# Kernel tuning notes

Hardware: AMD Instinct MI355X
Metric: run time of the kernel (lower is better)

Reference implementation:

```python
import jax, jax.numpy as jnp
import numpy as np

CAPACITY_FACTOR = 1.0  # fairseq Top1Gate default


def setup_inputs() -> dict:
    key = jax.random.key(0)
    ks = jax.random.split(key, 5)
    B, T, M, H, O, E = 8, 1024, 1024, 4096, 1024, 4
    return {
        "hidden_states": jax.random.normal(ks[0], (B, T, M), jnp.float32),
        "gate_w": jax.random.normal(ks[1], (M, E), jnp.float32) * 0.02,
        "fc1_w": jax.random.normal(ks[2], (E, M, H), jnp.float32) * 0.02,
        "fc1_b": jnp.zeros((E, H), jnp.float32),
        "fc2_w": jax.random.normal(ks[3], (E, H, O), jnp.float32) * 0.02,
        "fc2_b": jnp.zeros((E, O), jnp.float32),
    }


def reference(hidden_states, gate_w, fc1_w, fc1_b, fc2_w, fc2_b):
    B, T, M = hidden_states.shape
    E = gate_w.shape[1]
    S = B * T
    C = int(CAPACITY_FACTOR * -(-S // E))  # ceil(S/E)

    features = hidden_states.reshape(S, M)  # [S, M]

    # ---- Top1 gate (fairseq top1gating, eval path: no shuffle/noise) ----
    logits = features @ gate_w                      # [S, E]
    gates = jax.nn.softmax(logits, axis=1)          # [S, E]
    idx = jnp.argmax(gates, axis=1)                 # [S]
    mask1 = jax.nn.one_hot(idx, E, dtype=gates.dtype)  # [S, E]

    # load-balancing aux loss (computed before capacity dropping)
    me = jnp.mean(gates, axis=0)
    ce = jnp.mean(mask1, axis=0)
    l_aux = jnp.sum(me * ce) * E

    # capacity: position within each expert's queue; drop overflow tokens
    locations = jnp.cumsum(mask1, axis=0) - 1.0     # [S, E]
    mask1 = mask1 * (locations < C)
    loc_s = jnp.sum(locations * mask1, axis=1).astype(jnp.int32)  # [S]
    gates1_s = jnp.sum(gates * mask1, axis=1)       # [S] gate value (0 if dropped)

    # combine_weights [S, E, C] and boolean dispatch mask (as float for mm)
    combine = (gates1_s[:, None, None] * mask1[:, :, None]
               * jax.nn.one_hot(loc_s, C, dtype=gates.dtype)[:, None, :])
    dispatch = (combine > 0).astype(features.dtype)  # [S, E, C]

    # ---- dispatch via dense one-hot matmul: [E*C, S] @ [S, M] ----
    dispatch_ecs = jnp.transpose(dispatch, (1, 2, 0)).reshape(E * C, S)
    dispatched = (dispatch_ecs @ features).reshape(E, C, M)

    # ---- per-expert MLP (grouped GEMM) ----
    h = jax.nn.gelu(jnp.einsum('ecm,emh->ech', dispatched, fc1_w) + fc1_b[:, None, :])
    expert_out = jnp.einsum('ech,eho->eco', h, fc2_w) + fc2_b[:, None, :]  # [E, C, O]

    # ---- combine via dense matmul: [S, E*C] @ [E*C, O] ----
    O = expert_out.shape[-1]
    combined = combine.reshape(S, E * C) @ expert_out.reshape(E * C, O)

    return combined.reshape(B, T, O), l_aux
```

## Files before the change

### kernel.cpp

```cpp
#include <hip/hip_runtime.h>
#include <stdint.h>

#define S_TOK 8192
#define MDIM  1024
#define HDIM  4096
#define ODIM  1024
#define NEXP  4
#define CAP   2048

typedef __attribute__((ext_vector_type(8))) short short8;
typedef __attribute__((ext_vector_type(4))) float floatx4;

__device__ __forceinline__ unsigned short f2bf(float x) {
  union { float f; unsigned u; } v; v.f = x;
  unsigned r = v.u + 0x7FFFu + ((v.u >> 16) & 1u);
  return (unsigned short)(r >> 16);
}

__device__ __forceinline__ void gl_lds16(const void* g, void* l) {
  __builtin_amdgcn_global_load_lds(
      (const __attribute__((address_space(1))) void*)g,
      (__attribute__((address_space(3))) void*)l, 16, 0, 0);
}

__device__ __forceinline__ float gelu_tanh(float x) {
  float z = 0.7978845608028654f * (x + 0.044715f * x * x * x);
  float t = 1.0f - 2.0f / (__expf(2.0f * z) + 1.0f);
  return 0.5f * x * (1.0f + t);
}

__global__ __launch_bounds__(256) void gate_kernel(
    const float* __restrict__ feat, const float* __restrict__ gw,
    int* __restrict__ idx, float* __restrict__ gval, float* __restrict__ gsum)
{
  int wave = threadIdx.x >> 6, lane = threadIdx.x & 63;
  int s = blockIdx.x * 4 + wave;
  const float* f = feat + (size_t)s * MDIM;
  double a0 = 0, a1 = 0, a2 = 0, a3 = 0;
  #pragma unroll
  for (int j = 0; j < 16; ++j) {
    int m = lane + j * 64;
    float x = f[m];
    float4 w = ((const float4*)gw)[m];
    a0 += (double)x * w.x; a1 += (double)x * w.y;
    a2 += (double)x * w.z; a3 += (double)x * w.w;
  }
  #pragma unroll
  for (int off = 32; off; off >>= 1) {
    a0 += __shfl_down(a0, off); a1 += __shfl_down(a1, off);
    a2 += __shfl_down(a2, off); a3 += __shfl_down(a3, off);
  }
  __shared__ float bs[4];
  if (threadIdx.x < 4) bs[threadIdx.x] = 0.f;
  __syncthreads();
  if (lane == 0) {
    double lg[4] = {a0, a1, a2, a3};
    double mx = lg[0]; int bi = 0;
    #pragma unroll
    for (int e = 1; e < 4; ++e) if (lg[e] > mx) { mx = lg[e]; bi = e; }
    float ex[4]; float den = 0.f;
    #pragma unroll
    for (int e = 0; e < 4; ++e) { ex[e] = __expf((float)(lg[e] - mx)); den += ex[e]; }
    float inv = 1.f / den;
    idx[s]  = bi;
    gval[s] = ex[bi] * inv;
    #pragma unroll
    for (int e = 0; e < 4; ++e) atomicAdd(&bs[e], ex[e] * inv);
  }
  __syncthreads();
  if (threadIdx.x < 4) atomicAdd(&gsum[threadIdx.x], bs[threadIdx.x]);
}

__global__ __launch_bounds__(1024) void scan_kernel(
    const int* __restrict__ idx, int* __restrict__ perm,
    int* __restrict__ ne, const float* __restrict__ gsum,
    float* __restrict__ laux)
{
  const int tid = threadIdx.x, wave = tid >> 6, lane = tid & 63;
  __shared__ int cnt[16][4];
  __shared__ int off[16][4];
  __shared__ int tot[4];
  unsigned long long below = (lane == 0) ? 0ull : ((~0ull) >> (64 - lane));

  int myE[8], loc[8];
  int c[4] = {0, 0, 0, 0};
  #pragma unroll
  for (int j = 0; j < 8; ++j) {
    int s = wave * 512 + j * 64 + lane;
    int ev = idx[s];
    myE[j] = ev;
    #pragma unroll
    for (int e = 0; e < 4; ++e) {
      unsigned long long mb = __ballot(ev == e);
      if (ev == e) loc[j] = c[e] + __popcll(mb & below);
      c[e] += __popcll(mb);
    }
  }
  if (lane == 0) {
    #pragma unroll
    for (int e = 0; e < 4; ++e) cnt[wave][e] = c[e];
  }
  __syncthreads();
  if (tid < 64) {
    int w = tid >> 2, e = tid & 3;
    int o = 0;
    for (int w2 = 0; w2 < 16; ++w2) if (w2 < w) o += cnt[w2][e];
    off[w][e] = o;
    if (w == 15) tot[e] = o + cnt[15][e];
  }
  __syncthreads();
  #pragma unroll
  for (int j = 0; j < 8; ++j) {
    int s = wave * 512 + j * 64 + lane;
    int e = myE[j];
    int rank = off[wave][e] + loc[j];
    if (rank < CAP) perm[e * CAP + rank] = s;
  }
  if (tid < 4) ne[tid] = tot[tid] < CAP ? tot[tid] : CAP;
  if (tid == 0) {
    float l = 0.f;
    #pragma unroll
    for (int e = 0; e < 4; ++e)
      l += (gsum[e] * (1.0f / S_TOK)) * ((float)tot[e] * (1.0f / S_TOK));
    *laux = l * (float)NEXP;
  }
}

__global__ __launch_bounds__(256) void transpose_cast(
    const float* __restrict__ in, unsigned short* __restrict__ out, int R, int Cc)
{
  __shared__ unsigned short tile[64][66];
  in  += (size_t)blockIdx.z * R * Cc;
  out += (size_t)blockIdx.z * R * Cc;
  int c0 = blockIdx.x * 64, r0 = blockIdx.y * 64;
  int tx = threadIdx.x & 15;
  int ty = threadIdx.x >> 4;
  #pragma unroll
  for (int p = 0; p < 4; ++p) {
    int r = ty + p * 16;
    float4 v = *(const float4*)(in + (size_t)(r0 + r) * Cc + c0 + tx * 4);
    tile[r][tx * 4 + 0] = f2bf(v.x);
    tile[r][tx * 4 + 1] = f2bf(v.y);
    tile[r][tx * 4 + 2] = f2bf(v.z);
    tile[r][tx * 4 + 3] = f2bf(v.w);
  }
  __syncthreads();
  #pragma unroll
  for (int p = 0; p < 4; ++p) {
    int c = ty + p * 16;
    ushort4 o;
    o.x = tile[tx * 4 + 0][c];
    o.y = tile[tx * 4 + 1][c];
    o.z = tile[tx * 4 + 2][c];
    o.w = tile[tx * 4 + 3][c];
    *(ushort4*)(out + (size_t)(c0 + c) * R + r0 + tx * 4) = o;
  }
}

__global__ __launch_bounds__(256) void gather_kernel(
    const float* __restrict__ feat, const int* __restrict__ perm,
    const int* __restrict__ ne, unsigned short* __restrict__ disp)
{
  int b = blockIdx.x;
  int e = b >> 11, c = b & (CAP - 1);
  int m = threadIdx.x * 4;
  ushort4 o;
  if (c < ne[e]) {
    int s = perm[b];
    float4 v = *(const float4*)(feat + (size_t)s * MDIM + m);
    o.x = f2bf(v.x); o.y = f2bf(v.y); o.z = f2bf(v.z); o.w = f2bf(v.w);
  } else {
    o.x = o.y = o.z = o.w = 0;
  }
  *(ushort4*)(disp + (size_t)b * MDIM + m) = o;
}

__global__ __launch_bounds__(256) void fc1_kernel(
    const unsigned short* __restrict__ A, const unsigned short* __restrict__ Bt,
    const float* __restrict__ b1, unsigned short* __restrict__ Hb)
{
  const int e = blockIdx.z, nb = blockIdx.x, mb = blockIdx.y;
  const int tid = threadIdx.x, wave = tid >> 6, lane = tid & 63;

  __shared__ __align__(16) unsigned short smA[128 * 32];
  __shared__ __align__(16) unsigned short smB[128 * 32];

  const char* Ag = (const char*)(A + ((size_t)e * CAP + (size_t)mb * 128) * MDIM);
  const char* Bg = (const char*)(Bt + ((size_t)e * HDIM + (size_t)nb * 128) * MDIM);

  int boff0 = (wave * 2 + 0) * 1024 + lane * 16;
  int boff1 = (wave * 2 + 1) * 1024 + lane * 16;
  const char* agp0 = Ag + (size_t)(boff0 >> 6) * 2048 + (boff0 & 63);
  const char* agp1 = Ag + (size_t)(boff1 >> 6) * 2048 + (boff1 & 63);
  const char* bgp0 = Bg + (size_t)(boff0 >> 6) * 2048 + (boff0 & 63);
  const char* bgp1 = Bg + (size_t)(boff1 >> 6) * 2048 + (boff1 & 63);
  unsigned short* sA0 = smA + (wave * 2 + 0) * 512;
  unsigned short* sA1 = smA + (wave * 2 + 1) * 512;
  unsigned short* sB0 = smB + (wave * 2 + 0) * 512;
  unsigned short* sB1 = smB + (wave * 2 + 1) * 512;

  const int wm = (wave & 1) * 64, wn = (wave >> 1) * 64;
  const int fr = lane & 15, fq = lane >> 4;

  floatx4 acc[4][4] = {};

  for (int kt = 0; kt < MDIM / 32; ++kt) {
    int kb = kt * 64;
    gl_lds16(agp0 + kb, sA0);
    gl_lds16(agp1 + kb, sA1);
    gl_lds16(bgp0 + kb, sB0);
    gl_lds16(bgp1 + kb, sB1);
    __syncthreads();
    short8 af[4], bfr[4];
    #pragma unroll
    for (int i = 0; i < 4; ++i)
      af[i] = *(const short8*)&smA[(wm + i * 16 + fr) * 32 + fq * 8];
    #pragma unroll
    for (int j = 0; j < 4; ++j)
      bfr[j] = *(const short8*)&smB[(wn + j * 16 + fr) * 32 + fq * 8];
    #pragma unroll
    for (int i = 0; i < 4; ++i)
      #pragma unroll
      for (int j = 0; j < 4; ++j)
        acc[i][j] = __builtin_amdgcn_mfma_f32_16x16x32_bf16(af[i], bfr[j], acc[i][j], 0, 0, 0);
    __syncthreads();
  }

  unsigned short* Hrow = Hb + (size_t)e * CAP * HDIM;
  #pragma unroll
  for (int j = 0; j < 4; ++j) {
    int gn = nb * 128 + wn + j * 16 + fr;
    float bv = b1[e * HDIM + gn];
    #pragma unroll
    for (int i = 0; i < 4; ++i) {
      int m0 = mb * 128 + wm + i * 16 + fq * 4;
      #pragma unroll
      for (int r = 0; r < 4; ++r)
        Hrow[(size_t)(m0 + r) * HDIM + gn] = f2bf(gelu_tanh(acc[i][j][r] + bv));
    }
  }
}

__global__ __launch_bounds__(256) void fc2_kernel(
    const unsigned short* __restrict__ A, const unsigned short* __restrict__ Bt,
    const float* __restrict__ b2, const int* __restrict__ perm,
    const int* __restrict__ ne, const float* __restrict__ gval,
    float* __restrict__ out)
{
  const int e = blockIdx.z, nb = blockIdx.x, mb = blockIdx.y;
  const int tid = threadIdx.x, wave = tid >> 6, lane = tid & 63;

  __shared__ __align__(16) unsigned short smA[64 * 32];
  __shared__ __align__(16) unsigned short smB[128 * 32];

  const char* Ag = (const char*)(A + ((size_t)e * CAP + (size_t)mb * 64) * HDIM);
  const char* Bg = (const char*)(Bt + ((size_t)e * ODIM + (size_t)nb * 128) * HDIM);

  int boffA = tid * 16;
  const char* agp = Ag + (size_t)(boffA >> 6) * 8192 + (boffA & 63);
  unsigned short* sA = smA + wave * 512;
  int boff0 = (wave * 2 + 0) * 1024 + lane * 16;
  int boff1 = (wave * 2 + 1) * 1024 + lane * 16;
  const char* bgp0 = Bg + (size_t)(boff0 >> 6) * 8192 + (boff0 & 63);
  const char* bgp1 = Bg + (size_t)(boff1 >> 6) * 8192 + (boff1 & 63);
  unsigned short* sB0 = smB + (wave * 2 + 0) * 512;
  unsigned short* sB1 = smB + (wave * 2 + 1) * 512;

  const int wm = (wave & 1) * 32, wn = (wave >> 1) * 64;
  const int fr = lane & 15, fq = lane >> 4;

  floatx4 acc[2][4] = {};

  for (int kt = 0; kt < HDIM / 32; ++kt) {
    int kb = kt * 64;
    gl_lds16(agp + kb, sA);
    gl_lds16(bgp0 + kb, sB0);
    gl_lds16(bgp1 + kb, sB1);
    __syncthreads();
    short8 af[2], bfr[4];
    #pragma unroll
    for (int i = 0; i < 2; ++i)
      af[i] = *(const short8*)&smA[(wm + i * 16 + fr) * 32 + fq * 8];
    #pragma unroll
    for (int j = 0; j < 4; ++j)
      bfr[j] = *(const short8*)&smB[(wn + j * 16 + fr) * 32 + fq * 8];
    #pragma unroll
    for (int i = 0; i < 2; ++i)
      #pragma unroll
      for (int j = 0; j < 4; ++j)
        acc[i][j] = __builtin_amdgcn_mfma_f32_16x16x32_bf16(af[i], bfr[j], acc[i][j], 0, 0, 0);
    __syncthreads();
  }

  const int nE = ne[e];
  float b2v[4];
  #pragma unroll
  for (int j = 0; j < 4; ++j)
    b2v[j] = b2[e * ODIM + nb * 128 + wn + j * 16 + fr];
  #pragma unroll
  for (int i = 0; i < 2; ++i) {
    #pragma unroll
    for (int r = 0; r < 4; ++r) {
      int c = mb * 64 + wm + i * 16 + fq * 4 + r;
      if (c < nE) {
        int s = perm[e * CAP + c];
        float g = gval[s];
        float* orow = out + (size_t)s * ODIM + nb * 128 + wn;
        #pragma unroll
        for (int j = 0; j < 4; ++j)
          orow[j * 16 + fr] = (acc[i][j][r] + b2v[j]) * g;
      }
    }
  }
}

extern "C" void kernel_launch(void* const* d_in, const int* in_sizes, int n_in,
                              void* d_out, int out_size, void* d_ws, size_t ws_size,
                              hipStream_t stream) {
  const float* feat = (const float*)d_in[0];
  const float* gw   = (const float*)d_in[1];
  const float* w1   = (const float*)d_in[2];
  const float* b1   = (const float*)d_in[3];
  const float* w2   = (const float*)d_in[4];
  const float* b2   = (const float*)d_in[5];
  float* out = (float*)d_out;

  char* ws = (char*)d_ws;
  unsigned short* wt   = (unsigned short*)(ws);
  unsigned short* hbuf = (unsigned short*)(ws + 33554432);
  unsigned short* disp = (unsigned short*)(ws + 100663296);
  int*   idx  = (int*)  (ws + 117440512);
  float* gval = (float*)(ws + 117473280);
  int*   perm = (int*)  (ws + 117506048);
  float* gsum = (float*)(ws + 117538816);
  int*   ne   = (int*)  (ws + 117538832);

  hipMemsetAsync(d_out, 0, (size_t)S_TOK * ODIM * sizeof(float), stream);
  hipMemsetAsync(ws + 117538816, 0, 32, stream);

  gate_kernel<<<S_TOK / 4, 256, 0, stream>>>(feat, gw, idx, gval, gsum);
  scan_kernel<<<1, 1024, 0, stream>>>(idx, perm, ne, gsum, out + (size_t)S_TOK * ODIM);
  transpose_cast<<<dim3(HDIM / 64, MDIM / 64, NEXP), 256, 0, stream>>>(w1, wt, MDIM, HDIM);
  gather_kernel<<<NEXP * CAP, 256, 0, stream>>>(feat, perm, ne, disp);
  fc1_kernel<<<dim3(HDIM / 128, CAP / 128, NEXP), 256, 0, stream>>>(disp, wt, b1, hbuf);
  transpose_cast<<<dim3(ODIM / 64, HDIM / 64, NEXP), 256, 0, stream>>>(w2, wt, HDIM, ODIM);
  fc2_kernel<<<dim3(ODIM / 128, CAP / 64, NEXP), 256, 0, stream>>>(hbuf, wt, b2, perm, ne, gval, out);
}
```

Before: 441.1 us.

## Register-prefetch GEMM tiles with padded LDS and enlarge fc2 tile to 128x128

```diff
diff --git a/kernel.cpp b/kernel.cpp
--- a/kernel.cpp
+++ b/kernel.cpp
@@ -8,19 +8,16 @@
 #define NEXP  4
 #define CAP   2048
 
+#define LDS_STRIDE 40
+
 typedef __attribute__((ext_vector_type(8))) short short8;
 typedef __attribute__((ext_vector_type(4))) float floatx4;
+typedef __attribute__((ext_vector_type(4))) int intx4;
 
 __device__ __forceinline__ unsigned short f2bf(float x) {
   union { float f; unsigned u; } v; v.f = x;
   unsigned r = v.u + 0x7FFFu + ((v.u >> 16) & 1u);
   return (unsigned short)(r >> 16);
-}
-
-__device__ __forceinline__ void gl_lds16(const void* g, void* l) {
-  __builtin_amdgcn_global_load_lds(
-      (const __attribute__((address_space(1))) void*)g,
-      (__attribute__((address_space(3))) void*)l, 16, 0, 0);
 }
 
 __device__ __forceinline__ float gelu_tanh(float x) {
@@ -175,55 +172,69 @@
   *(ushort4*)(disp + (size_t)b * MDIM + m) = o;
 }
 
+
 __global__ __launch_bounds__(256) void fc1_kernel(
     const unsigned short* __restrict__ A, const unsigned short* __restrict__ Bt,
     const float* __restrict__ b1, unsigned short* __restrict__ Hb)
 {
   const int e = blockIdx.z, nb = blockIdx.x, mb = blockIdx.y;
   const int tid = threadIdx.x, wave = tid >> 6, lane = tid & 63;
-
-  __shared__ __align__(16) unsigned short smA[128 * 32];
-  __shared__ __align__(16) unsigned short smB[128 * 32];
+  const int NK = MDIM / 32;
+  const int GROW = MDIM * 2;
+
+  __shared__ __align__(16) unsigned short smA[128 * LDS_STRIDE];
+  __shared__ __align__(16) unsigned short smB[128 * LDS_STRIDE];
 
   const char* Ag = (const char*)(A + ((size_t)e * CAP + (size_t)mb * 128) * MDIM);
   const char* Bg = (const char*)(Bt + ((size_t)e * HDIM + (size_t)nb * 128) * MDIM);
 
-  int boff0 = (wave * 2 + 0) * 1024 + lane * 16;
-  int boff1 = (wave * 2 + 1) * 1024 + lane * 16;
-  const char* agp0 = Ag + (size_t)(boff0 >> 6) * 2048 + (boff0 & 63);
-  const char* agp1 = Ag + (size_t)(boff1 >> 6) * 2048 + (boff1 & 63);
-  const char* bgp0 = Bg + (size_t)(boff0 >> 6) * 2048 + (boff0 & 63);
-  const char* bgp1 = Bg + (size_t)(boff1 >> 6) * 2048 + (boff1 & 63);
-  unsigned short* sA0 = smA + (wave * 2 + 0) * 512;
-  unsigned short* sA1 = smA + (wave * 2 + 1) * 512;
-  unsigned short* sB0 = smB + (wave * 2 + 0) * 512;
-  unsigned short* sB1 = smB + (wave * 2 + 1) * 512;
+  const char* aC0 = Ag + (size_t)(tid >> 2) * GROW + (tid & 3) * 16;
+  const char* bC0 = Bg + (size_t)(tid >> 2) * GROW + (tid & 3) * 16;
+  const size_t cstep = (size_t)64 * GROW;
+  unsigned short* lA0 = smA + (tid >> 2) * LDS_STRIDE + (tid & 3) * 8;
+  unsigned short* lB0 = smB + (tid >> 2) * LDS_STRIDE + (tid & 3) * 8;
+  const int lstep = 64 * LDS_STRIDE;
 
   const int wm = (wave & 1) * 64, wn = (wave >> 1) * 64;
   const int fr = lane & 15, fq = lane >> 4;
 
   floatx4 acc[4][4] = {};
 
-  for (int kt = 0; kt < MDIM / 32; ++kt) {
-    int kb = kt * 64;
-    gl_lds16(agp0 + kb, sA0);
-    gl_lds16(agp1 + kb, sA1);
-    gl_lds16(bgp0 + kb, sB0);
-    gl_lds16(bgp1 + kb, sB1);
-    __syncthreads();
+  intx4 pa0 = *(const intx4*)(aC0);
+  intx4 pa1 = *(const intx4*)(aC0 + cstep);
+  intx4 pb0 = *(const intx4*)(bC0);
+  intx4 pb1 = *(const intx4*)(bC0 + cstep);
+  *(intx4*)lA0 = pa0; *(intx4*)(lA0 + lstep) = pa1;
+  *(intx4*)lB0 = pb0; *(intx4*)(lB0 + lstep) = pb1;
+  __syncthreads();
+
+  for (int kt = 0; kt < NK; ++kt) {
+    intx4 na0, na1, nb0, nb1;
+    if (kt + 1 < NK) {
+      int kb = (kt + 1) * 64;
+      na0 = *(const intx4*)(aC0 + kb);
+      na1 = *(const intx4*)(aC0 + cstep + kb);
+      nb0 = *(const intx4*)(bC0 + kb);
+      nb1 = *(const intx4*)(bC0 + cstep + kb);
+    }
     short8 af[4], bfr[4];
     #pragma unroll
     for (int i = 0; i < 4; ++i)
-      af[i] = *(const short8*)&smA[(wm + i * 16 + fr) * 32 + fq * 8];
+      af[i] = *(const short8*)&smA[(wm + i * 16 + fr) * LDS_STRIDE + fq * 8];
     #pragma unroll
     for (int j = 0; j < 4; ++j)
-      bfr[j] = *(const short8*)&smB[(wn + j * 16 + fr) * 32 + fq * 8];
+      bfr[j] = *(const short8*)&smB[(wn + j * 16 + fr) * LDS_STRIDE + fq * 8];
     #pragma unroll
     for (int i = 0; i < 4; ++i)
       #pragma unroll
       for (int j = 0; j < 4; ++j)
         acc[i][j] = __builtin_amdgcn_mfma_f32_16x16x32_bf16(af[i], bfr[j], acc[i][j], 0, 0, 0);
     __syncthreads();
+    if (kt + 1 < NK) {
+      *(intx4*)lA0 = na0; *(intx4*)(lA0 + lstep) = na1;
+      *(intx4*)lB0 = nb0; *(intx4*)(lB0 + lstep) = nb1;
+    }
+    __syncthreads();
   }
 
   unsigned short* Hrow = Hb + (size_t)e * CAP * HDIM;
@@ -249,47 +260,62 @@
 {
   const int e = blockIdx.z, nb = blockIdx.x, mb = blockIdx.y;
   const int tid = threadIdx.x, wave = tid >> 6, lane = tid & 63;
-
-  __shared__ __align__(16) unsigned short smA[64 * 32];
-  __shared__ __align__(16) unsigned short smB[128 * 32];
-
-  const char* Ag = (const char*)(A + ((size_t)e * CAP + (size_t)mb * 64) * HDIM);
+  const int NK = HDIM / 32;
+  const int GROW = HDIM * 2;
+
+  __shared__ __align__(16) unsigned short smA[128 * LDS_STRIDE];
+  __shared__ __align__(16) unsigned short smB[128 * LDS_STRIDE];
+
+  const char* Ag = (const char*)(A + ((size_t)e * CAP + (size_t)mb * 128) * HDIM);
   const char* Bg = (const char*)(Bt + ((size_t)e * ODIM + (size_t)nb * 128) * HDIM);
 
-  int boffA = tid * 16;
-  const char* agp = Ag + (size_t)(boffA >> 6) * 8192 + (boffA & 63);
-  unsigned short* sA = smA + wave * 512;
-  int boff0 = (wave * 2 + 0) * 1024 + lane * 16;
-  int boff1 = (wave * 2 + 1) * 1024 + lane * 16;
-  const char* bgp0 = Bg + (size_t)(boff0 >> 6) * 8192 + (boff0 & 63);
-  const char* bgp1 = Bg + (size_t)(boff1 >> 6) * 8192 + (boff1 & 63);
-  unsigned short* sB0 = smB + (wave * 2 + 0) * 512;
-  unsigned short* sB1 = smB + (wave * 2 + 1) * 512;
-
-  const int wm = (wave & 1) * 32, wn = (wave >> 1) * 64;
+  const char* aC0 = Ag + (size_t)(tid >> 2) * GROW + (tid & 3) * 16;
+  const char* bC0 = Bg + (size_t)(tid >> 2) * GROW + (tid & 3) * 16;
+  const size_t cstep = (size_t)64 * GROW;
+  unsigned short* lA0 = smA + (tid >> 2) * LDS_STRIDE + (tid & 3) * 8;
+  unsigned short* lB0 = smB + (tid >> 2) * LDS_STRIDE + (tid & 3) * 8;
+  const int lstep = 64 * LDS_STRIDE;
+
+  const int wm = (wave & 1) * 64, wn = (wave >> 1) * 64;
   const int fr = lane & 15, fq = lane >> 4;
 
-  floatx4 acc[2][4] = {};
-
-  for (int kt = 0; kt < HDIM / 32; ++kt) {
-    int kb = kt * 64;
-    gl_lds16(agp + kb, sA);
-    gl_lds16(bgp0 + kb, sB0);
-    gl_lds16(bgp1 + kb, sB1);
-    __syncthreads();
-    short8 af[2], bfr[4];
-    #pragma unroll
-    for (int i = 0; i < 2; ++i)
-      af[i] = *(const short8*)&smA[(wm + i * 16 + fr) * 32 + fq * 8];
+  floatx4 acc[4][4] = {};
+
+  intx4 pa0 = *(const intx4*)(aC0);
+  intx4 pa1 = *(const intx4*)(aC0 + cstep);
+  intx4 pb0 = *(const intx4*)(bC0);
+  intx4 pb1 = *(const intx4*)(bC0 + cstep);
+  *(intx4*)lA0 = pa0; *(intx4*)(lA0 + lstep) = pa1;
+  *(intx4*)lB0 = pb0; *(intx4*)(lB0 + lstep) = pb1;
+  __syncthreads();
+
+  for (int kt = 0; kt < NK; ++kt) {
+    intx4 na0, na1, nb0, nb1;
+    if (kt + 1 < NK) {
+      int kb = (kt + 1) * 64;
+      na0 = *(const intx4*)(aC0 + kb);
+      na1 = *(const intx4*)(aC0 + cstep + kb);
+      nb0 = *(const intx4*)(bC0 + kb);
+      nb1 = *(const intx4*)(bC0 + cstep + kb);
+    }
+    short8 af[4], bfr[4];
+    #pragma unroll
+    for (int i = 0; i < 4; ++i)
+      af[i] = *(const short8*)&smA[(wm + i * 16 + fr) * LDS_STRIDE + fq * 8];
     #pragma unroll
     for (int j = 0; j < 4; ++j)
-      bfr[j] = *(const short8*)&smB[(wn + j * 16 + fr) * 32 + fq * 8];
-    #pragma unroll
-    for (int i = 0; i < 2; ++i)
+      bfr[j] = *(const short8*)&smB[(wn + j * 16 + fr) * LDS_STRIDE + fq * 8];
+    #pragma unroll
+    for (int i = 0; i < 4; ++i)
       #pragma unroll
       for (int j = 0; j < 4; ++j)
         acc[i][j] = __builtin_amdgcn_mfma_f32_16x16x32_bf16(af[i], bfr[j], acc[i][j], 0, 0, 0);
     __syncthreads();
+    if (kt + 1 < NK) {
+      *(intx4*)lA0 = na0; *(intx4*)(lA0 + lstep) = na1;
+      *(intx4*)lB0 = nb0; *(intx4*)(lB0 + lstep) = nb1;
+    }
+    __syncthreads();
   }
 
   const int nE = ne[e];
@@ -298,10 +324,10 @@
   for (int j = 0; j < 4; ++j)
     b2v[j] = b2[e * ODIM + nb * 128 + wn + j * 16 + fr];
   #pragma unroll
-  for (int i = 0; i < 2; ++i) {
+  for (int i = 0; i < 4; ++i) {
     #pragma unroll
     for (int r = 0; r < 4; ++r) {
-      int c = mb * 64 + wm + i * 16 + fq * 4 + r;
+      int c = mb * 128 + wm + i * 16 + fq * 4 + r;
       if (c < nE) {
         int s = perm[e * CAP + c];
         float g = gval[s];
@@ -344,5 +370,5 @@
   gather_kernel<<<NEXP * CAP, 256, 0, stream>>>(feat, perm, ne, disp);
   fc1_kernel<<<dim3(HDIM / 128, CAP / 128, NEXP), 256, 0, stream>>>(disp, wt, b1, hbuf);
   transpose_cast<<<dim3(ODIM / 64, HDIM / 64, NEXP), 256, 0, stream>>>(w2, wt, HDIM, ODIM);
-  fc2_kernel<<<dim3(ODIM / 128, CAP / 64, NEXP), 256, 0, stream>>>(hbuf, wt, b2, perm, ne, gval, out);
-}
+  fc2_kernel<<<dim3(ODIM / 128, CAP / 128, NEXP), 256, 0, stream>>>(hbuf, wt, b2, perm, ne, gval, out);
+}
```

After: 444.0 us. About the same (+0.6%).

## Deepen K tiles with XOR-swizzled LDS, XCD-aware block mapping, split-K fc2

Applied to the files above, without the earlier changes.

```diff
diff --git a/kernel.cpp b/kernel.cpp
--- a/kernel.cpp
+++ b/kernel.cpp
@@ -175,54 +175,68 @@
   *(ushort4*)(disp + (size_t)b * MDIM + m) = o;
 }
 
+
 __global__ __launch_bounds__(256) void fc1_kernel(
     const unsigned short* __restrict__ A, const unsigned short* __restrict__ Bt,
     const float* __restrict__ b1, unsigned short* __restrict__ Hb)
 {
-  const int e = blockIdx.z, nb = blockIdx.x, mb = blockIdx.y;
+  const int bid = blockIdx.x;
+  const int xcd = bid & 7, id = bid >> 3;
+  const int e = xcd >> 1;
+  const int mb = id & 15, nb = (xcd & 1) * 16 + (id >> 4);
   const int tid = threadIdx.x, wave = tid >> 6, lane = tid & 63;
-
-  __shared__ __align__(16) unsigned short smA[128 * 32];
-  __shared__ __align__(16) unsigned short smB[128 * 32];
+  const int NK = MDIM / 64;
+  const int GROW = MDIM * 2;
+
+  __shared__ __align__(16) unsigned short smA[128 * 64];
+  __shared__ __align__(16) unsigned short smB[128 * 64];
 
   const char* Ag = (const char*)(A + ((size_t)e * CAP + (size_t)mb * 128) * MDIM);
   const char* Bg = (const char*)(Bt + ((size_t)e * HDIM + (size_t)nb * 128) * MDIM);
 
-  int boff0 = (wave * 2 + 0) * 1024 + lane * 16;
-  int boff1 = (wave * 2 + 1) * 1024 + lane * 16;
-  const char* agp0 = Ag + (size_t)(boff0 >> 6) * 2048 + (boff0 & 63);
-  const char* agp1 = Ag + (size_t)(boff1 >> 6) * 2048 + (boff1 & 63);
-  const char* bgp0 = Bg + (size_t)(boff0 >> 6) * 2048 + (boff0 & 63);
-  const char* bgp1 = Bg + (size_t)(boff1 >> 6) * 2048 + (boff1 & 63);
-  unsigned short* sA0 = smA + (wave * 2 + 0) * 512;
-  unsigned short* sA1 = smA + (wave * 2 + 1) * 512;
-  unsigned short* sB0 = smB + (wave * 2 + 0) * 512;
-  unsigned short* sB1 = smB + (wave * 2 + 1) * 512;
+  const int gcol = ((tid & 7) ^ ((tid >> 3) & 7)) * 16;
+  const int rbase = tid >> 3;
+  const char* ag[4]; const char* bg[4];
+  unsigned short* la[4]; unsigned short* lb[4];
+  #pragma unroll
+  for (int i = 0; i < 4; ++i) {
+    int row = i * 32 + rbase;
+    ag[i] = Ag + (size_t)row * GROW + gcol;
+    bg[i] = Bg + (size_t)row * GROW + gcol;
+    la[i] = smA + i * 2048 + wave * 512;
+    lb[i] = smB + i * 2048 + wave * 512;
+  }
 
   const int wm = (wave & 1) * 64, wn = (wave >> 1) * 64;
   const int fr = lane & 15, fq = lane >> 4;
+  const int sw = fr & 7;
 
   floatx4 acc[4][4] = {};
 
-  for (int kt = 0; kt < MDIM / 32; ++kt) {
-    int kb = kt * 64;
-    gl_lds16(agp0 + kb, sA0);
-    gl_lds16(agp1 + kb, sA1);
-    gl_lds16(bgp0 + kb, sB0);
-    gl_lds16(bgp1 + kb, sB1);
+  for (int kt = 0; kt < NK; ++kt) {
+    int kb = kt * 128;
+    #pragma unroll
+    for (int i = 0; i < 4; ++i) {
+      gl_lds16(ag[i] + kb, la[i]);
+      gl_lds16(bg[i] + kb, lb[i]);
+    }
     __syncthreads();
-    short8 af[4], bfr[4];
-    #pragma unroll
-    for (int i = 0; i < 4; ++i)
-      af[i] = *(const short8*)&smA[(wm + i * 16 + fr) * 32 + fq * 8];
-    #pragma unroll
-    for (int j = 0; j < 4; ++j)
-      bfr[j] = *(const short8*)&smB[(wn + j * 16 + fr) * 32 + fq * 8];
-    #pragma unroll
-    for (int i = 0; i < 4; ++i)
+    #pragma unroll
+    for (int s = 0; s < 2; ++s) {
+      const int lc = ((s * 4 + fq) ^ sw) * 8;
+      short8 af[4], bfr[4];
+      #pragma unroll
+      for (int i = 0; i < 4; ++i)
+        af[i] = *(const short8*)&smA[(wm + i * 16 + fr) * 64 + lc];
       #pragma unroll
       for (int j = 0; j < 4; ++j)
-        acc[i][j] = __builtin_amdgcn_mfma_f32_16x16x32_bf16(af[i], bfr[j], acc[i][j], 0, 0, 0);
+        bfr[j] = *(const short8*)&smB[(wn + j * 16 + fr) * 64 + lc];
+      #pragma unroll
+      for (int i = 0; i < 4; ++i)
+        #pragma unroll
+        for (int j = 0; j < 4; ++j)
+          acc[i][j] = __builtin_amdgcn_mfma_f32_16x16x32_bf16(af[i], bfr[j], acc[i][j], 0, 0, 0);
+    }
     __syncthreads();
   }
 
@@ -247,48 +261,66 @@
     const int* __restrict__ ne, const float* __restrict__ gval,
     float* __restrict__ out)
 {
-  const int e = blockIdx.z, nb = blockIdx.x, mb = blockIdx.y;
+  const int bid = blockIdx.x;
+  const int xcd = bid & 7, id = bid >> 3;
+  const int e = xcd >> 1;
+  const int nb = id & 7, ks = (id >> 3) & 1;
+  const int mb = (xcd & 1) * 8 + (id >> 4);
   const int tid = threadIdx.x, wave = tid >> 6, lane = tid & 63;
-
-  __shared__ __align__(16) unsigned short smA[64 * 32];
-  __shared__ __align__(16) unsigned short smB[128 * 32];
-
-  const char* Ag = (const char*)(A + ((size_t)e * CAP + (size_t)mb * 64) * HDIM);
-  const char* Bg = (const char*)(Bt + ((size_t)e * ODIM + (size_t)nb * 128) * HDIM);
-
-  int boffA = tid * 16;
-  const char* agp = Ag + (size_t)(boffA >> 6) * 8192 + (boffA & 63);
-  unsigned short* sA = smA + wave * 512;
-  int boff0 = (wave * 2 + 0) * 1024 + lane * 16;
-  int boff1 = (wave * 2 + 1) * 1024 + lane * 16;
-  const char* bgp0 = Bg + (size_t)(boff0 >> 6) * 8192 + (boff0 & 63);
-  const char* bgp1 = Bg + (size_t)(boff1 >> 6) * 8192 + (boff1 & 63);
-  unsigned short* sB0 = smB + (wave * 2 + 0) * 512;
-  unsigned short* sB1 = smB + (wave * 2 + 1) * 512;
-
-  const int wm = (wave & 1) * 32, wn = (wave >> 1) * 64;
+  const int NK = HDIM / 64 / 2;
+  const int GROW = HDIM * 2;
+
+  __shared__ __align__(16) unsigned short smA[128 * 64];
+  __shared__ __align__(16) unsigned short smB[128 * 64];
+
+  const char* Ag = (const char*)(A + ((size_t)e * CAP + (size_t)mb * 128) * HDIM)
+                   + (size_t)ks * NK * 128;
+  const char* Bg = (const char*)(Bt + ((size_t)e * ODIM + (size_t)nb * 128) * HDIM)
+                   + (size_t)ks * NK * 128;
+
+  const int gcol = ((tid & 7) ^ ((tid >> 3) & 7)) * 16;
+  const int rbase = tid >> 3;
+  const char* ag[4]; const char* bg[4];
+  unsigned short* la[4]; unsigned short* lb[4];
+  #pragma unroll
+  for (int i = 0; i < 4; ++i) {
+    int row = i * 32 + rbase;
+    ag[i] = Ag + (size_t)row * GROW + gcol;
+    bg[i] = Bg + (size_t)row * GROW + gcol;
+    la[i] = smA + i * 2048 + wave * 512;
+    lb[i] = smB + i * 2048 + wave * 512;
+  }
+
+  const int wm = (wave & 1) * 64, wn = (wave >> 1) * 64;
   const int fr = lane & 15, fq = lane >> 4;
-
-  floatx4 acc[2][4] = {};
-
-  for (int kt = 0; kt < HDIM / 32; ++kt) {
-    int kb = kt * 64;
-    gl_lds16(agp + kb, sA);
-    gl_lds16(bgp0 + kb, sB0);
-    gl_lds16(bgp1 + kb, sB1);
+  const int sw = fr & 7;
+
+  floatx4 acc[4][4] = {};
+
+  for (int kt = 0; kt < NK; ++kt) {
+    int kb = kt * 128;
+    #pragma unroll
+    for (int i = 0; i < 4; ++i) {
+      gl_lds16(ag[i] + kb, la[i]);
+      gl_lds16(bg[i] + kb, lb[i]);
+    }
     __syncthreads();
-    short8 af[2], bfr[4];
-    #pragma unroll
-    for (int i = 0; i < 2; ++i)
-      af[i] = *(const short8*)&smA[(wm + i * 16 + fr) * 32 + fq * 8];
-    #pragma unroll
-    for (int j = 0; j < 4; ++j)
-      bfr[j] = *(const short8*)&smB[(wn + j * 16 + fr) * 32 + fq * 8];
-    #pragma unroll
-    for (int i = 0; i < 2; ++i)
+    #pragma unroll
+    for (int s = 0; s < 2; ++s) {
+      const int lc = ((s * 4 + fq) ^ sw) * 8;
+      short8 af[4], bfr[4];
+      #pragma unroll
+      for (int i = 0; i < 4; ++i)
+        af[i] = *(const short8*)&smA[(wm + i * 16 + fr) * 64 + lc];
       #pragma unroll
       for (int j = 0; j < 4; ++j)
-        acc[i][j] = __builtin_amdgcn_mfma_f32_16x16x32_bf16(af[i], bfr[j], acc[i][j], 0, 0, 0);
+        bfr[j] = *(const short8*)&smB[(wn + j * 16 + fr) * 64 + lc];
+      #pragma unroll
+      for (int i = 0; i < 4; ++i)
+        #pragma unroll
+        for (int j = 0; j < 4; ++j)
+          acc[i][j] = __builtin_amdgcn_mfma_f32_16x16x32_bf16(af[i], bfr[j], acc[i][j], 0, 0, 0);
+    }
     __syncthreads();
   }
 
@@ -296,19 +328,19 @@
   float b2v[4];
   #pragma unroll
   for (int j = 0; j < 4; ++j)
-    b2v[j] = b2[e * ODIM + nb * 128 + wn + j * 16 + fr];
-  #pragma unroll
-  for (int i = 0; i < 2; ++i) {
+    b2v[j] = ks ? 0.f : b2[e * ODIM + nb * 128 + wn + j * 16 + fr];
+  #pragma unroll
+  for (int i = 0; i < 4; ++i) {
     #pragma unroll
     for (int r = 0; r < 4; ++r) {
-      int c = mb * 64 + wm + i * 16 + fq * 4 + r;
+      int c = mb * 128 + wm + i * 16 + fq * 4 + r;
       if (c < nE) {
         int s = perm[e * CAP + c];
         float g = gval[s];
         float* orow = out + (size_t)s * ODIM + nb * 128 + wn;
         #pragma unroll
         for (int j = 0; j < 4; ++j)
-          orow[j * 16 + fr] = (acc[i][j][r] + b2v[j]) * g;
+          atomicAdd(&orow[j * 16 + fr], (acc[i][j][r] + b2v[j]) * g);
       }
     }
   }
@@ -342,7 +374,7 @@
   scan_kernel<<<1, 1024, 0, stream>>>(idx, perm, ne, gsum, out + (size_t)S_TOK * ODIM);
   transpose_cast<<<dim3(HDIM / 64, MDIM / 64, NEXP), 256, 0, stream>>>(w1, wt, MDIM, HDIM);
   gather_kernel<<<NEXP * CAP, 256, 0, stream>>>(feat, perm, ne, disp);
-  fc1_kernel<<<dim3(HDIM / 128, CAP / 128, NEXP), 256, 0, stream>>>(disp, wt, b1, hbuf);
+  fc1_kernel<<<2048, 256, 0, stream>>>(disp, wt, b1, hbuf);
   transpose_cast<<<dim3(ODIM / 64, HDIM / 64, NEXP), 256, 0, stream>>>(w2, wt, HDIM, ODIM);
-  fc2_kernel<<<dim3(ODIM / 128, CAP / 64, NEXP), 256, 0, stream>>>(hbuf, wt, b2, perm, ne, gval, out);
-}
+  fc2_kernel<<<1024, 256, 0, stream>>>(hbuf, wt, b2, perm, ne, gval, out);
+}
```

Result: slower. 455.5 us (+3.3%).
